# Kernel tuning notes

Measured on AMD Instinct MI355X. Metric: run time of the kernel, lower is better.

Reference implementation:

```python
import jax, jax.numpy as jnp
import numpy as np

NUM_HEADS = 12
WINDOW = 14  # window size == input_size[0]; rel pos tables are (2*WINDOW-1, head_dim)


def setup_inputs() -> dict:
    key = jax.random.key(0)
    ks = jax.random.split(key, 6)
    C = 768
    x = jax.random.normal(ks[0], (16, 56, 56, C), dtype=jnp.float32)
    qkv_w = jax.random.normal(ks[1], (3 * C, C), dtype=jnp.float32) * 0.02
    qkv_b = jnp.zeros((3 * C,), dtype=jnp.float32)
    proj_w = jax.random.normal(ks[2], (C, C), dtype=jnp.float32) * 0.02
    proj_b = jnp.zeros((C,), dtype=jnp.float32)
    hd = C // NUM_HEADS
    rel_pos_h = jax.random.normal(ks[3], (2 * WINDOW - 1, hd), dtype=jnp.float32) * 0.02
    rel_pos_w = jax.random.normal(ks[4], (2 * WINDOW - 1, hd), dtype=jnp.float32) * 0.02
    return {"x": x, "qkv_w": qkv_w, "qkv_b": qkv_b, "proj_w": proj_w,
            "proj_b": proj_b, "rel_pos_h": rel_pos_h, "rel_pos_w": rel_pos_w}


def reference(x, qkv_w, qkv_b, proj_w, proj_b, rel_pos_h, rel_pos_w):
    B, H, W, C = x.shape
    nh, ws = NUM_HEADS, WINDOW
    hd = C // nh
    scale = hd ** -0.5
    # --- window_partition (H, W divisible by ws -> no padding branch) ---
    xw = x.reshape(B, H // ws, ws, W // ws, ws, C)
    xw = xw.transpose(0, 1, 3, 2, 4, 5).reshape(-1, ws * ws, C)  # (Bw, N, C)
    Bw, N, _ = xw.shape
    # --- qkv projection ---
    qkv = xw @ qkv_w.T + qkv_b  # (Bw, N, 3C)
    qkv = qkv.reshape(Bw, N, 3, nh, hd).transpose(2, 0, 3, 1, 4)
    qkv = qkv.reshape(3, Bw * nh, N, hd)
    q, k, v = qkv[0], qkv[1], qkv[2]
    # --- scaled attention scores ---
    attn = jnp.einsum('bqd,bkd->bqk', q * scale, k)  # (Bw*nh, N, N)
    # --- decomposed relative position bias (q_size == k_size == ws) ---
    idx = jnp.arange(ws)[:, None] - jnp.arange(ws)[None, :] + (ws - 1)
    Rh = rel_pos_h[idx]  # (ws, ws, hd)
    Rw = rel_pos_w[idx]  # (ws, ws, hd)
    rq = q.reshape(Bw * nh, ws, ws, hd)
    rel_h = jnp.einsum('bhwc,hkc->bhwk', rq, Rh)
    rel_w = jnp.einsum('bhwc,wkc->bhwk', rq, Rw)
    attn = (attn.reshape(Bw * nh, ws, ws, ws, ws)
            + rel_h[:, :, :, :, None] + rel_w[:, :, :, None, :])
    attn = jax.nn.softmax(attn.reshape(Bw * nh, N, N), axis=-1)
    # --- weighted values + output projection ---
    out = jnp.einsum('bqk,bkd->bqd', attn, v)
    out = out.reshape(Bw, nh, ws, ws, hd).transpose(0, 2, 3, 1, 4).reshape(Bw, ws, ws, C)
    out = out @ proj_w.T + proj_b
    # --- window_unpartition ---
    out = out.reshape(B, H // ws, W // ws, ws, ws, C)
    out = out.transpose(0, 1, 3, 2, 4, 5).reshape(B, H, W, C)
    return out
```

## Files before the change

### kernel.cpp

```cpp
#include <hip/hip_runtime.h>
#include <stdint.h>

typedef __bf16 bfv8 __attribute__((ext_vector_type(8)));
typedef short s16x8 __attribute__((ext_vector_type(8)));
typedef short s16x4 __attribute__((ext_vector_type(4)));
typedef float f32x4 __attribute__((ext_vector_type(4)));
typedef float f32x16 __attribute__((ext_vector_type(16)));

#define MFMA(a, b, c) __builtin_amdgcn_mfma_f32_16x16x32_bf16(a, b, c, 0, 0, 0)
#define MFMA32(a, b, c) __builtin_amdgcn_mfma_f32_32x32x16_bf16(a, b, c, 0, 0, 0)

__device__ __forceinline__ short f2bf(float f) {
  union { float f; unsigned u; } v; v.f = f;
  unsigned r = v.u + 0x7FFFu + ((v.u >> 16) & 1u);
  return (short)(r >> 16);
}
__device__ __forceinline__ float bf2f(short s) {
  union { unsigned u; float f; } v; v.u = ((unsigned)(unsigned short)s) << 16;
  return v.f;
}
__device__ __forceinline__ unsigned pack2(float a, float b) {
  return (unsigned)(unsigned short)f2bf(a) | ((unsigned)(unsigned short)f2bf(b) << 16);
}
__device__ __forceinline__ bfv8 mkfrag(unsigned a, unsigned b, unsigned c, unsigned d) {
  union { unsigned u[4]; bfv8 v; } t; t.u[0] = a; t.u[1] = b; t.u[2] = c; t.u[3] = d;
  return t.v;
}

__device__ __forceinline__ void async_cp16(const short* g, short* l) {
  auto gp = reinterpret_cast<const uint32_t __attribute__((address_space(1)))*>(
      reinterpret_cast<uintptr_t>(g));
  auto lp = reinterpret_cast<uint32_t __attribute__((address_space(3)))*>(
      reinterpret_cast<uintptr_t>(l));
  __builtin_amdgcn_global_load_lds(gp, lp, 16, 0, 0);
}

__global__ __launch_bounds__(256) void convert_all(
    const float* __restrict__ x, const float* __restrict__ qkvw,
    const float* __restrict__ projw, const float* __restrict__ rph,
    const float* __restrict__ rpw, short* __restrict__ Xbf,
    short* __restrict__ Wq, short* __restrict__ Wp, short* __restrict__ Rhb,
    short* __restrict__ Rwb) {
  const int NX = 9633792;
  const int NW1 = 442368;
  const int NW2 = 147456;
  const int NR = 512;
  int idx = blockIdx.x * 256 + threadIdx.x;
  if (idx < NX) {
    int t = idx / 192, cq = idx - t * 192;
    int wdx = t / 196, n = t - wdx * 196;
    int b = wdx >> 4, wl = wdx & 15;
    int nh = n / 14;
    int hh = (wl >> 2) * 14 + nh;
    int ww = (wl & 3) * 14 + (n - nh * 14);
    float4 v = *(const float4*)(x + ((b * 56 + hh) * 56 + ww) * 768 + cq * 4);
    s16x4 s = {f2bf(v.x), f2bf(v.y), f2bf(v.z), f2bf(v.w)};
    *(s16x4*)(Xbf + idx * 4) = s;
  } else if (idx < NX + NW1) {
    int i = idx - NX;
    float4 v = ((const float4*)qkvw)[i];
    s16x4 s = {f2bf(v.x), f2bf(v.y), f2bf(v.z), f2bf(v.w)};
    *(s16x4*)(Wq + i * 4) = s;
  } else if (idx < NX + NW1 + NW2) {
    int i = idx - NX - NW1;
    float4 v = ((const float4*)projw)[i];
    s16x4 s = {f2bf(v.x), f2bf(v.y), f2bf(v.z), f2bf(v.w)};
    *(s16x4*)(Wp + i * 4) = s;
  } else if (idx < NX + NW1 + NW2 + 2 * NR) {
    int i = idx - NX - NW1 - NW2;
    int which = i >> 9;
    int j = i & 511;
    int p = j >> 4, q = j & 15;
    const float* src = which ? rpw : rph;
    short* dst = which ? Rwb : Rhb;
    s16x4 s = {0, 0, 0, 0};
    if (p < 27) {
      float4 v = *(const float4*)(src + p * 64 + q * 4);
      s = (s16x4){f2bf(v.x), f2bf(v.y), f2bf(v.z), f2bf(v.w)};
    }
    *(s16x4*)(dst + p * 64 + q * 4) = s;
  }
}

__global__ __launch_bounds__(256) void qkv_gemm(
    const short* __restrict__ Xbf, const short* __restrict__ Wq,
    const float* __restrict__ qkvb, short* __restrict__ Q,
    short* __restrict__ K, short* __restrict__ V) {
  __shared__ short As[128 * 32];
  __shared__ short Bs[128 * 32];
  int bid = blockIdx.x;
  int wg = (bid & 7) * 882 + (bid >> 3);
  int bm = wg / 18, bn = wg - bm * 18;
  const int tid = threadIdx.x, lane = tid & 63, wave = tid >> 6;
  const int row0 = (wave >> 1) * 64, col0 = (wave & 1) * 64;
  const int li = lane & 15, g8 = (lane >> 4) * 8;

  const int c0 = wave * 2;
  const int rr = c0 * 16 + (lane >> 2);
  const int seg = (lane & 3) * 8;
  const short* asrc = Xbf + (bm * 128 + rr) * 768 + seg;
  const short* bsrc = Wq + (bn * 128 + rr) * 768 + seg;
  short* alds0 = As + c0 * 512;
  short* alds1 = As + c0 * 512 + 512;
  short* blds0 = Bs + c0 * 512;
  short* blds1 = Bs + c0 * 512 + 512;

  f32x4 acc[4][4];
#pragma unroll
  for (int i = 0; i < 4; ++i)
#pragma unroll
    for (int j = 0; j < 4; ++j) acc[i][j] = (f32x4){0.f, 0.f, 0.f, 0.f};

  for (int k0 = 0; k0 < 768; k0 += 32) {
    async_cp16(asrc + k0, alds0);
    async_cp16(asrc + 16 * 768 + k0, alds1);
    async_cp16(bsrc + k0, blds0);
    async_cp16(bsrc + 16 * 768 + k0, blds1);
    __syncthreads();
    bfv8 af[4], bfr[4];
#pragma unroll
    for (int mi = 0; mi < 4; ++mi)
      af[mi] = *(const bfv8*)&As[(row0 + mi * 16 + li) * 32 + g8];
#pragma unroll
    for (int ni = 0; ni < 4; ++ni)
      bfr[ni] = *(const bfv8*)&Bs[(col0 + ni * 16 + li) * 32 + g8];
#pragma unroll
    for (int mi = 0; mi < 4; ++mi)
#pragma unroll
      for (int ni = 0; ni < 4; ++ni)
        acc[mi][ni] = MFMA(af[mi], bfr[ni], acc[mi][ni]);
    __syncthreads();
  }

  const int g4 = (lane >> 4) * 4;
#pragma unroll
  for (int mi = 0; mi < 4; ++mi) {
    int rbase = bm * 128 + row0 + mi * 16 + g4;
#pragma unroll
    for (int ni = 0; ni < 4; ++ni) {
      int col = bn * 128 + col0 + ni * 16 + li;
      int which = col / 768;
      int cm = col - which * 768;
      int head = cm >> 6, d = cm & 63;
      short* dst = (which == 0) ? Q : ((which == 1) ? K : V);
      float bias = qkvb[col];
      f32x4 a = acc[mi][ni];
#pragma unroll
      for (int j = 0; j < 4; ++j) {
        int t = rbase + j;
        int wdx = t / 196, n = t - wdx * 196;
        dst[((wdx * 12 + head) * 196 + n) * 64 + d] = f2bf(a[j] + bias);
      }
    }
  }
}

__global__ __launch_bounds__(512, 4) void attn_kernel(
    const short* __restrict__ Q, const short* __restrict__ K,
    const short* __restrict__ V, const short* __restrict__ Rhb,
    const short* __restrict__ Rwb, short* __restrict__ AO) {
  __shared__ short Ks[196 * 64];
  __shared__ short Vt[64 * 204];
  __shared__ short relh[224 * 28];
  __shared__ short relw[224 * 28];
  __shared__ short2 hw[224];

  const int bh = blockIdx.x;
  const int wdx = bh / 12, head = bh - wdx * 12;
  const int tid = threadIdx.x, lane = tid & 63, wave = tid >> 6;
  const int l31 = lane & 31, hb = lane >> 5;
  const short* Qb = Q + bh * 12544;
  const short* Kb = K + bh * 12544;
  const short* Vb = V + bh * 12544;

  const int m0 = wave * 32;
  const int qv = (m0 + l31 > 195) ? 195 : m0 + l31;

  bfv8 qf[4];
  if (wave < 7) {
    f32x16 ra = {0.f, 0.f, 0.f, 0.f, 0.f, 0.f, 0.f, 0.f,
                 0.f, 0.f, 0.f, 0.f, 0.f, 0.f, 0.f, 0.f};
    f32x16 rw_ = ra;
#pragma unroll
    for (int s = 0; s < 4; ++s) {
      qf[s] = *(const bfv8*)(Qb + qv * 64 + s * 16 + hb * 8);
      ra = MFMA32(*(const bfv8*)(Rhb + l31 * 64 + s * 16 + hb * 8), qf[s], ra);
      rw_ = MFMA32(*(const bfv8*)(Rwb + l31 * 64 + s * 16 + hb * 8), qf[s], rw_);
    }
#pragma unroll
    for (int reg = 0; reg < 16; ++reg) {
      int p = (reg & 3) + 8 * (reg >> 2) + 4 * hb;
      if (!(hb && reg >= 12)) {
        relh[(m0 + l31) * 28 + p] = f2bf(ra[reg]);
        relw[(m0 + l31) * 28 + p] = f2bf(rw_[reg]);
      }
    }
  }

  if (tid < 64) {
    s16x8 z = {0, 0, 0, 0, 0, 0, 0, 0};
    *(s16x8*)&Vt[tid * 204 + 196] = z;
  }
  for (int c = tid; c < 1568; c += 512) {
    int r = c >> 3, cc = c & 7;
    s16x8 v = *(const s16x8*)(Kb + r * 64 + cc * 8);
    *(s16x8*)&Ks[r * 64 + (((cc ^ (r & 7))) << 3)] = v;
  }
  for (int t = tid; t < 784; t += 512) {
    int dseg = t / 98, kp = t - dseg * 98, d0 = dseg * 8;
    s16x8 a = *(const s16x8*)(Vb + (2 * kp) * 64 + d0);
    s16x8 b = *(const s16x8*)(Vb + (2 * kp + 1) * 64 + d0);
#pragma unroll
    for (int i = 0; i < 8; ++i)
      *(short2*)&Vt[(d0 + i) * 204 + 2 * kp] = make_short2(a[i], b[i]);
  }
  if (tid < 224) {
    int kc = (tid > 195) ? 195 : tid;
    int hk = kc / 14, wk = kc - hk * 14;
    hw[tid] = make_short2((short)(13 - hk), (short)(13 - wk));
  }
  __syncthreads();

  if (wave >= 7) return;

  const int hq = qv / 14;
  const int wq = qv - hq * 14;
  const short* relhq = &relh[qv * 28 + hq];
  const short* relwq = &relw[qv * 28 + wq];

  f32x16 oacc0 = {0.f, 0.f, 0.f, 0.f, 0.f, 0.f, 0.f, 0.f,
                  0.f, 0.f, 0.f, 0.f, 0.f, 0.f, 0.f, 0.f};
  f32x16 oacc1 = oacc0;
  float psum = 0.f;

#pragma unroll
  for (int nt = 0; nt < 7; ++nt) {
    int krow = nt * 32 + l31;
    int krc = (krow > 195) ? 195 : krow;
    const int rb = krc * 64, rx = krc & 7;
    f32x16 st = {0.f, 0.f, 0.f, 0.f, 0.f, 0.f, 0.f, 0.f,
                 0.f, 0.f, 0.f, 0.f, 0.f, 0.f, 0.f, 0.f};
#pragma unroll
    for (int s = 0; s < 4; ++s) {
      bfv8 kf = *(const bfv8*)&Ks[rb + (((2 * s + hb) ^ rx) << 3)];
      st = MFMA32(kf, qf[s], st);
    }
    float pv[16];
    float lsum = 0.f;
#pragma unroll
    for (int reg = 0; reg < 16; ++reg) {
      int koff = (reg & 3) + 8 * (reg >> 2) + 4 * hb;
      int k = nt * 32 + koff;
      short2 dxy = hw[k];
      float b = bf2f(relhq[dxy.x]) + bf2f(relwq[dxy.y]);
      float sv = fmaf(st[reg], 0.125f, b);
      float e = __expf(sv);
      if (nt == 6) {
        if (reg >= 4) e = 0.f;
        else if (hb) e = 0.f;
      }
      pv[reg] = e;
      lsum += e;
    }
    psum += lsum;
    unsigned pk[8], xk[8];
#pragma unroll
    for (int i = 0; i < 8; ++i) pk[i] = pack2(pv[2 * i], pv[2 * i + 1]);
#pragma unroll
    for (int i = 0; i < 8; ++i) xk[i] = (unsigned)__shfl_xor((int)pk[i], 32);

    {
      bfv8 pf = mkfrag(hb ? xk[2] : pk[0], hb ? xk[3] : pk[1],
                       hb ? pk[2] : xk[0], hb ? pk[3] : xk[1]);
      int kb = nt * 32 + hb * 8;
      if (nt == 6 && hb) kb = 0;
      oacc0 = MFMA32(pf, *(const bfv8*)&Vt[l31 * 204 + kb], oacc0);
      oacc1 = MFMA32(pf, *(const bfv8*)&Vt[(32 + l31) * 204 + kb], oacc1);
    }
    {
      bfv8 pf = mkfrag(hb ? xk[6] : pk[4], hb ? xk[7] : pk[5],
                       hb ? pk[6] : xk[4], hb ? pk[7] : xk[5]);
      int kb = nt * 32 + 16 + hb * 8;
      if (nt == 6) kb = 0;
      oacc0 = MFMA32(pf, *(const bfv8*)&Vt[l31 * 204 + kb], oacc0);
      oacc1 = MFMA32(pf, *(const bfv8*)&Vt[(32 + l31) * 204 + kb], oacc1);
    }
  }

  float inv = 1.f / (psum + __shfl_xor(psum, 32));
  short* AOr = AO + (wdx * 196) * 768 + head * 64;
#pragma unroll
  for (int reg = 0; reg < 16; ++reg) {
    int qoff = (reg & 3) + 8 * (reg >> 2) + 4 * hb;
    float invr = __shfl(inv, qoff);
    int q = m0 + qoff;
    if (q < 196) {
      AOr[q * 768 + l31] = f2bf(oacc0[reg] * invr);
      AOr[q * 768 + 32 + l31] = f2bf(oacc1[reg] * invr);
    }
  }
}

__global__ __launch_bounds__(256) void proj_gemm(
    const short* __restrict__ AO, const short* __restrict__ Wp,
    const float* __restrict__ projb, float* __restrict__ out) {
  __shared__ short As[128 * 32];
  __shared__ short Bs[128 * 32];
  int bid = blockIdx.x;
  int wg = (bid & 7) * 294 + (bid >> 3);
  int bm = wg / 6, bn = wg - bm * 6;
  const int tid = threadIdx.x, lane = tid & 63, wave = tid >> 6;
  const int row0 = (wave >> 1) * 64, col0 = (wave & 1) * 64;
  const int li = lane & 15, g8 = (lane >> 4) * 8;

  const int c0 = wave * 2;
  const int rr = c0 * 16 + (lane >> 2);
  const int seg = (lane & 3) * 8;
  const short* asrc = AO + (bm * 128 + rr) * 768 + seg;
  const short* bsrc = Wp + (bn * 128 + rr) * 768 + seg;
  short* alds0 = As + c0 * 512;
  short* alds1 = As + c0 * 512 + 512;
  short* blds0 = Bs + c0 * 512;
  short* blds1 = Bs + c0 * 512 + 512;

  f32x4 acc[4][4];
#pragma unroll
  for (int i = 0; i < 4; ++i)
#pragma unroll
    for (int j = 0; j < 4; ++j) acc[i][j] = (f32x4){0.f, 0.f, 0.f, 0.f};

  for (int k0 = 0; k0 < 768; k0 += 32) {
    async_cp16(asrc + k0, alds0);
    async_cp16(asrc + 16 * 768 + k0, alds1);
    async_cp16(bsrc + k0, blds0);
    async_cp16(bsrc + 16 * 768 + k0, blds1);
    __syncthreads();
    bfv8 af[4], bfr[4];
#pragma unroll
    for (int mi = 0; mi < 4; ++mi)
      af[mi] = *(const bfv8*)&As[(row0 + mi * 16 + li) * 32 + g8];
#pragma unroll
    for (int ni = 0; ni < 4; ++ni)
      bfr[ni] = *(const bfv8*)&Bs[(col0 + ni * 16 + li) * 32 + g8];
#pragma unroll
    for (int mi = 0; mi < 4; ++mi)
#pragma unroll
      for (int ni = 0; ni < 4; ++ni)
        acc[mi][ni] = MFMA(af[mi], bfr[ni], acc[mi][ni]);
    __syncthreads();
  }

  const int g4 = (lane >> 4) * 4;
#pragma unroll
  for (int mi = 0; mi < 4; ++mi) {
    int rbase = bm * 128 + row0 + mi * 16 + g4;
#pragma unroll
    for (int ni = 0; ni < 4; ++ni) {
      int col = bn * 128 + col0 + ni * 16 + li;
      float bias = projb[col];
      f32x4 a = acc[mi][ni];
#pragma unroll
      for (int j = 0; j < 4; ++j) {
        int t = rbase + j;
        int wdx = t / 196, n = t - wdx * 196;
        int b = wdx >> 4, wl = wdx & 15;
        int nh = n / 14;
        int hh = (wl >> 2) * 14 + nh;
        int ww = (wl & 3) * 14 + (n - nh * 14);
        out[((b * 56 + hh) * 56 + ww) * 768 + col] = a[j] + bias;
      }
    }
  }
}

extern "C" void kernel_launch(void* const* d_in, const int* in_sizes, int n_in,
                              void* d_out, int out_size, void* d_ws, size_t ws_size,
                              hipStream_t stream) {
  const float* x = (const float*)d_in[0];
  const float* qkv_w = (const float*)d_in[1];
  const float* qkv_b = (const float*)d_in[2];
  const float* proj_w = (const float*)d_in[3];
  const float* proj_b = (const float*)d_in[4];
  const float* rph = (const float*)d_in[5];
  const float* rpw = (const float*)d_in[6];
  float* out = (float*)d_out;

  char* ws = (char*)d_ws;
  short* Q  = (short*)(ws);
  short* K  = (short*)(ws + 77070336);
  short* V  = (short*)(ws + 154140672);
  short* AO = (short*)(ws + 231211008);
  short* Wq = (short*)(ws + 308281344);
  short* Wp = (short*)(ws + 311820288);
  short* Xbf = (short*)d_out;
  short* Rhb = (short*)((char*)d_out + 77070336);
  short* Rwb = Rhb + 2048;

  hipLaunchKernelGGL(convert_all, dim3(39940), dim3(256), 0, stream,
                     x, qkv_w, proj_w, rph, rpw, Xbf, Wq, Wp, Rhb, Rwb);
  hipLaunchKernelGGL(qkv_gemm, dim3(7056), dim3(256), 0, stream,
                     Xbf, Wq, qkv_b, Q, K, V);
  hipLaunchKernelGGL(attn_kernel, dim3(3072), dim3(512), 0, stream,
                     Q, K, V, Rhb, Rwb, AO);
  hipLaunchKernelGGL(proj_gemm, dim3(2352), dim3(256), 0, stream,
                     AO, Wp, proj_b, out);
}
```

Before: 531.1 us.

## Rewrite QKV and projection GEMMs with 256x256 tiles, double-buffered swizzled LDS

Both GEMMs move from 128x128 tiles with 32-deep K steps and 256 threads to 256x256 tiles with 64-deep K steps and 512 threads. Global-to-LDS copies are double-buffered so the next stage loads while the current one computes, and LDS columns are XOR-swizzled to avoid bank conflicts. MFMA issue is raised in priority, and the XCD workgroup remap and epilogue stores are adjusted for the new grid. This cuts global re-reads and synchronisation per FLOP, at the cost of higher register and LDS use (128KB per block) and fewer blocks in flight.

```diff
diff --git a/kernel.cpp b/kernel.cpp
--- a/kernel.cpp
+++ b/kernel.cpp
@@ -82,75 +82,139 @@
   }
 }
 
-__global__ __launch_bounds__(256) void qkv_gemm(
+
+#define GEMM_PRE()                                                            \
+  const int tid = threadIdx.x, lane = tid & 63, w = tid >> 6;                 \
+  const int wr = w >> 2, wc = w & 3;                                          \
+  const int li = lane & 15, g = lane >> 4;                                    \
+  const int lr = lane >> 3, ls = lane & 7;                                    \
+  const int ss = ls ^ lr;                                                     \
+  f32x4 acc[8][4];                                                            \
+  _Pragma("unroll") for (int i = 0; i < 8; ++i)                               \
+  _Pragma("unroll") for (int j = 0; j < 4; ++j)                               \
+      acc[i][j] = (f32x4){0.f, 0.f, 0.f, 0.f};
+
+#define GEMM_STAGE(buf, t)                                                    \
+  {                                                                           \
+    _Pragma("unroll") for (int q = 0; q < 4; ++q) {                           \
+      async_cp16(Asrc + q * 8 * 768 + (t) * 64, &As[buf][(w * 32 + q * 8) * 64]); \
+      async_cp16(Bsrc + q * 8 * 768 + (t) * 64, &Bs[buf][(w * 32 + q * 8) * 64]); \
+    }                                                                         \
+  }
+
+#define GEMM_WAITBAR()                                                        \
+  asm volatile("s_waitcnt vmcnt(0)" ::: "memory");                            \
+  __builtin_amdgcn_sched_barrier(0);                                          \
+  __builtin_amdgcn_s_barrier();
+
+#define GEMM_COMPUTE(buf)                                                     \
+  {                                                                           \
+    const short* Ab = As[buf];                                                \
+    const short* Bb = Bs[buf];                                                \
+    bfv8 bfr[4][2];                                                           \
+    _Pragma("unroll") for (int nf = 0; nf < 4; ++nf)                          \
+    _Pragma("unroll") for (int kh = 0; kh < 2; ++kh)                          \
+        bfr[nf][kh] = *(const bfv8*)&Bb[(wc * 64 + nf * 16 + li) * 64 +       \
+                                        (((kh * 4 + g) ^ (li & 7)) * 8)];     \
+    _Pragma("unroll") for (int mh = 0; mh < 2; ++mh) {                        \
+      bfv8 af[4][2];                                                          \
+      _Pragma("unroll") for (int mf = 0; mf < 4; ++mf)                        \
+      _Pragma("unroll") for (int kh = 0; kh < 2; ++kh)                        \
+          af[mf][kh] = *(const bfv8*)&Ab[(wr * 128 + mh * 64 + mf * 16 + li) * 64 + \
+                                         (((kh * 4 + g) ^ (li & 7)) * 8)];    \
+      __builtin_amdgcn_s_setprio(1);                                          \
+      _Pragma("unroll") for (int mf = 0; mf < 4; ++mf)                        \
+      _Pragma("unroll") for (int nf = 0; nf < 4; ++nf) {                      \
+        acc[mh * 4 + mf][nf] = MFMA(af[mf][0], bfr[nf][0], acc[mh * 4 + mf][nf]); \
+        acc[mh * 4 + mf][nf] = MFMA(af[mf][1], bfr[nf][1], acc[mh * 4 + mf][nf]); \
+      }                                                                       \
+      __builtin_amdgcn_s_setprio(0);                                          \
+    }                                                                         \
+  }
+
+#define GEMM_LOOP()                                                           \
+  GEMM_STAGE(0, 0);                                                           \
+  _Pragma("unroll 1") for (int tt = 0; tt < 6; ++tt) {                        \
+    GEMM_WAITBAR();                                                           \
+    GEMM_STAGE(1, 2 * tt + 1);                                                \
+    GEMM_COMPUTE(0);                                                          \
+    GEMM_WAITBAR();                                                           \
+    if (tt < 5) GEMM_STAGE(0, 2 * tt + 2);                                    \
+    GEMM_COMPUTE(1);                                                          \
+  }
+
+__global__ __launch_bounds__(512, 2) void qkv_gemm(
     const short* __restrict__ Xbf, const short* __restrict__ Wq,
     const float* __restrict__ qkvb, short* __restrict__ Q,
     short* __restrict__ K, short* __restrict__ V) {
-  __shared__ short As[128 * 32];
-  __shared__ short Bs[128 * 32];
+  __shared__ short As[2][256 * 64];
+  __shared__ short Bs[2][256 * 64];
   int bid = blockIdx.x;
-  int wg = (bid & 7) * 882 + (bid >> 3);
-  int bm = wg / 18, bn = wg - bm * 18;
-  const int tid = threadIdx.x, lane = tid & 63, wave = tid >> 6;
-  const int row0 = (wave >> 1) * 64, col0 = (wave & 1) * 64;
-  const int li = lane & 15, g8 = (lane >> 4) * 8;
-
-  const int c0 = wave * 2;
-  const int rr = c0 * 16 + (lane >> 2);
-  const int seg = (lane & 3) * 8;
-  const short* asrc = Xbf + (bm * 128 + rr) * 768 + seg;
-  const short* bsrc = Wq + (bn * 128 + rr) * 768 + seg;
-  short* alds0 = As + c0 * 512;
-  short* alds1 = As + c0 * 512 + 512;
-  short* blds0 = Bs + c0 * 512;
-  short* blds1 = Bs + c0 * 512 + 512;
-
-  f32x4 acc[4][4];
-#pragma unroll
-  for (int i = 0; i < 4; ++i)
-#pragma unroll
-    for (int j = 0; j < 4; ++j) acc[i][j] = (f32x4){0.f, 0.f, 0.f, 0.f};
-
-  for (int k0 = 0; k0 < 768; k0 += 32) {
-    async_cp16(asrc + k0, alds0);
-    async_cp16(asrc + 16 * 768 + k0, alds1);
-    async_cp16(bsrc + k0, blds0);
-    async_cp16(bsrc + 16 * 768 + k0, blds1);
-    __syncthreads();
-    bfv8 af[4], bfr[4];
-#pragma unroll
-    for (int mi = 0; mi < 4; ++mi)
-      af[mi] = *(const bfv8*)&As[(row0 + mi * 16 + li) * 32 + g8];
-#pragma unroll
-    for (int ni = 0; ni < 4; ++ni)
-      bfr[ni] = *(const bfv8*)&Bs[(col0 + ni * 16 + li) * 32 + g8];
-#pragma unroll
-    for (int mi = 0; mi < 4; ++mi)
-#pragma unroll
-      for (int ni = 0; ni < 4; ++ni)
-        acc[mi][ni] = MFMA(af[mi], bfr[ni], acc[mi][ni]);
-    __syncthreads();
-  }
-
-  const int g4 = (lane >> 4) * 4;
-#pragma unroll
-  for (int mi = 0; mi < 4; ++mi) {
-    int rbase = bm * 128 + row0 + mi * 16 + g4;
-#pragma unroll
-    for (int ni = 0; ni < 4; ++ni) {
-      int col = bn * 128 + col0 + ni * 16 + li;
-      int which = col / 768;
-      int cm = col - which * 768;
-      int head = cm >> 6, d = cm & 63;
-      short* dst = (which == 0) ? Q : ((which == 1) ? K : V);
-      float bias = qkvb[col];
-      f32x4 a = acc[mi][ni];
-#pragma unroll
-      for (int j = 0; j < 4; ++j) {
-        int t = rbase + j;
-        int wdx = t / 196, n = t - wdx * 196;
-        dst[((wdx * 12 + head) * 196 + n) * 64 + d] = f2bf(a[j] + bias);
-      }
+  int xcd = bid & 7, pos = bid >> 3;
+  int wgid = (xcd < 4) ? xcd * 221 + pos : 884 + (xcd - 4) * 220 + pos;
+  int bm = wgid / 9, bn = wgid - bm * 9;
+
+  GEMM_PRE();
+  const short* Asrc = Xbf + (bm * 256 + w * 32 + lr) * 768 + ss * 8;
+  const short* Bsrc = Wq + (bn * 256 + w * 32 + lr) * 768 + ss * 8;
+
+  GEMM_LOOP();
+
+  short* dst = (bn < 3) ? Q : ((bn < 6) ? K : V);
+  const int head = (bn % 3) * 4 + wc;
+  float bias[4];
+#pragma unroll
+  for (int nf = 0; nf < 4; ++nf) bias[nf] = qkvb[bn * 256 + wc * 64 + nf * 16 + li];
+#pragma unroll
+  for (int mi = 0; mi < 8; ++mi) {
+    int rbase = bm * 256 + wr * 128 + (mi >> 2) * 64 + (mi & 3) * 16 + g * 4;
+#pragma unroll
+    for (int j = 0; j < 4; ++j) {
+      int trow = rbase + j;
+      int wdx = trow / 196, n = trow - wdx * 196;
+      int base = ((wdx * 12 + head) * 196 + n) * 64;
+#pragma unroll
+      for (int nf = 0; nf < 4; ++nf)
+        dst[base + nf * 16 + li] = f2bf(acc[mi][nf][j] + bias[nf]);
+    }
+  }
+}
+
+__global__ __launch_bounds__(512, 2) void proj_gemm(
+    const short* __restrict__ AO, const short* __restrict__ Wp,
+    const float* __restrict__ projb, float* __restrict__ out) {
+  __shared__ short As[2][256 * 64];
+  __shared__ short Bs[2][256 * 64];
+  int bid = blockIdx.x;
+  int xcd = bid & 7, pos = bid >> 3;
+  int wgid = (xcd < 4) ? xcd * 74 + pos : 296 + (xcd - 4) * 73 + pos;
+  int bm = wgid / 3, bn = wgid - bm * 3;
+
+  GEMM_PRE();
+  const short* Asrc = AO + (bm * 256 + w * 32 + lr) * 768 + ss * 8;
+  const short* Bsrc = Wp + (bn * 256 + w * 32 + lr) * 768 + ss * 8;
+
+  GEMM_LOOP();
+
+  float bias[4];
+#pragma unroll
+  for (int nf = 0; nf < 4; ++nf) bias[nf] = projb[bn * 256 + wc * 64 + nf * 16 + li];
+  const int col0 = bn * 256 + wc * 64 + li;
+#pragma unroll
+  for (int mi = 0; mi < 8; ++mi) {
+    int rbase = bm * 256 + wr * 128 + (mi >> 2) * 64 + (mi & 3) * 16 + g * 4;
+#pragma unroll
+    for (int j = 0; j < 4; ++j) {
+      int trow = rbase + j;
+      int wdx = trow / 196, n = trow - wdx * 196;
+      int b = wdx >> 4, wl = wdx & 15;
+      int nh = n / 14;
+      int hh = (wl >> 2) * 14 + nh;
+      int ww = (wl & 3) * 14 + (n - nh * 14);
+      float* orow = out + ((b * 56 + hh) * 56 + ww) * 768 + col0;
+#pragma unroll
+      for (int nf = 0; nf < 4; ++nf)
+        orow[nf * 16] = acc[mi][nf][j] + bias[nf];
     }
   }
 }
@@ -301,78 +365,6 @@
   }
 }
 
-__global__ __launch_bounds__(256) void proj_gemm(
-    const short* __restrict__ AO, const short* __restrict__ Wp,
-    const float* __restrict__ projb, float* __restrict__ out) {
-  __shared__ short As[128 * 32];
-  __shared__ short Bs[128 * 32];
-  int bid = blockIdx.x;
-  int wg = (bid & 7) * 294 + (bid >> 3);
-  int bm = wg / 6, bn = wg - bm * 6;
-  const int tid = threadIdx.x, lane = tid & 63, wave = tid >> 6;
-  const int row0 = (wave >> 1) * 64, col0 = (wave & 1) * 64;
-  const int li = lane & 15, g8 = (lane >> 4) * 8;
-
-  const int c0 = wave * 2;
-  const int rr = c0 * 16 + (lane >> 2);
-  const int seg = (lane & 3) * 8;
-  const short* asrc = AO + (bm * 128 + rr) * 768 + seg;
-  const short* bsrc = Wp + (bn * 128 + rr) * 768 + seg;
-  short* alds0 = As + c0 * 512;
-  short* alds1 = As + c0 * 512 + 512;
-  short* blds0 = Bs + c0 * 512;
-  short* blds1 = Bs + c0 * 512 + 512;
-
-  f32x4 acc[4][4];
-#pragma unroll
-  for (int i = 0; i < 4; ++i)
-#pragma unroll
-    for (int j = 0; j < 4; ++j) acc[i][j] = (f32x4){0.f, 0.f, 0.f, 0.f};
-
-  for (int k0 = 0; k0 < 768; k0 += 32) {
-    async_cp16(asrc + k0, alds0);
-    async_cp16(asrc + 16 * 768 + k0, alds1);
-    async_cp16(bsrc + k0, blds0);
-    async_cp16(bsrc + 16 * 768 + k0, blds1);
-    __syncthreads();
-    bfv8 af[4], bfr[4];
-#pragma unroll
-    for (int mi = 0; mi < 4; ++mi)
-      af[mi] = *(const bfv8*)&As[(row0 + mi * 16 + li) * 32 + g8];
-#pragma unroll
-    for (int ni = 0; ni < 4; ++ni)
-      bfr[ni] = *(const bfv8*)&Bs[(col0 + ni * 16 + li) * 32 + g8];
-#pragma unroll
-    for (int mi = 0; mi < 4; ++mi)
-#pragma unroll
-      for (int ni = 0; ni < 4; ++ni)
-        acc[mi][ni] = MFMA(af[mi], bfr[ni], acc[mi][ni]);
-    __syncthreads();
-  }
-
-  const int g4 = (lane >> 4) * 4;
-#pragma unroll
-  for (int mi = 0; mi < 4; ++mi) {
-    int rbase = bm * 128 + row0 + mi * 16 + g4;
-#pragma unroll
-    for (int ni = 0; ni < 4; ++ni) {
-      int col = bn * 128 + col0 + ni * 16 + li;
-      float bias = projb[col];
-      f32x4 a = acc[mi][ni];
-#pragma unroll
-      for (int j = 0; j < 4; ++j) {
-        int t = rbase + j;
-        int wdx = t / 196, n = t - wdx * 196;
-        int b = wdx >> 4, wl = wdx & 15;
-        int nh = n / 14;
-        int hh = (wl >> 2) * 14 + nh;
-        int ww = (wl & 3) * 14 + (n - nh * 14);
-        out[((b * 56 + hh) * 56 + ww) * 768 + col] = a[j] + bias;
-      }
-    }
-  }
-}
-
 extern "C" void kernel_launch(void* const* d_in, const int* in_sizes, int n_in,
                               void* d_out, int out_size, void* d_ws, size_t ws_size,
                               hipStream_t stream) {
@@ -398,10 +390,10 @@
 
   hipLaunchKernelGGL(convert_all, dim3(39940), dim3(256), 0, stream,
                      x, qkv_w, proj_w, rph, rpw, Xbf, Wq, Wp, Rhb, Rwb);
-  hipLaunchKernelGGL(qkv_gemm, dim3(7056), dim3(256), 0, stream,
+  hipLaunchKernelGGL(qkv_gemm, dim3(1764), dim3(512), 0, stream,
                      Xbf, Wq, qkv_b, Q, K, V);
   hipLaunchKernelGGL(attn_kernel, dim3(3072), dim3(512), 0, stream,
                      Q, K, V, Rhb, Rwb, AO);
-  hipLaunchKernelGGL(proj_gemm, dim3(2352), dim3(256), 0, stream,
+  hipLaunchKernelGGL(proj_gemm, dim3(588), dim3(512), 0, stream,
                      AO, Wp, proj_b, out);
 }
```

After: 461.7 us. 13.1% less time.
